# Optimization experiments

Measured on AMD Instinct MI355X. Metric: run time of the kernel, lower is better.

The kernel has to match this reference:

```python
import jax, jax.numpy as jnp
import numpy as np

B, S, DX, DM, H = 4, 2048, 1024, 1024, 16
DK = DM // H


def setup_inputs() -> dict:
    key = jax.random.key(0)
    ks = jax.random.split(key, 12)
    s = 0.02
    inp = {
        "q": jax.random.normal(ks[0], (B, S, DX), jnp.float32),
        "k": jax.random.normal(ks[1], (B, S, DX), jnp.float32),
        "v": jax.random.normal(ks[2], (B, S, DX), jnp.float32),
        "wq": jax.random.normal(ks[3], (DX, DM), jnp.float32) * s,
        "bq": jnp.zeros((DM,), jnp.float32),
        "wk": jax.random.normal(ks[4], (DX, DM), jnp.float32) * s,
        "bk": jnp.zeros((DM,), jnp.float32),
        "wv": jax.random.normal(ks[5], (DX, DM), jnp.float32) * s,
        "bv": jnp.zeros((DM,), jnp.float32),
        "wo": jax.random.normal(ks[6], (DM, DX), jnp.float32) * s,
        "bo": jnp.zeros((DX,), jnp.float32),
        # causal boolean mask [B, S_q, S_k]; True = attend
        "mask": jnp.broadcast_to(jnp.tril(jnp.ones((S, S), bool)), (B, S, S)),
    }
    return inp


def reference(q, k, v, wq, bq, wk, bk, wv, bv, wo, bo, mask):
    # Linear projections: [B,S,DX] @ [DX,DM] -> [B,S,DM]
    qh = (q @ wq + bq).reshape(B, S, H, DK).transpose(0, 2, 1, 3)  # [B,H,S,DK]
    kh = (k @ wk + bk).reshape(B, S, H, DK).transpose(0, 2, 1, 3)
    vh = (v @ wv + bv).reshape(B, S, H, DK).transpose(0, 2, 1, 3)

    scores = jnp.einsum("bhqd,bhkd->bhqk", qh, kh) / jnp.sqrt(jnp.float32(DK))
    neg = -jnp.finfo(scores.dtype).max
    scores = jnp.where(mask[:, None, :, :], scores, neg)  # mask.unsqueeze(1)
    p = jax.nn.softmax(scores, axis=-1)  # dropout inactive (eval / p=0)
    z = jnp.einsum("bhqk,bhkd->bhqd", p, vh)  # [B,H,S,DK]
    z = z.transpose(0, 2, 1, 3).reshape(B, S, DM)
    return z @ wo + bo
```

## Files before the change

### kernel.cpp

```cpp
#include <hip/hip_runtime.h>
#include <hip/hip_bf16.h>
#include <cstdint>

constexpr int Bb = 4, Sq = 2048, DXc = 1024, DMc = 1024, NH = 16, DKc = 64;
constexpr int GM = Bb * Sq;

typedef __attribute__((ext_vector_type(8))) short short8;
typedef __attribute__((ext_vector_type(4))) float f32x4;

__device__ inline float b2f(unsigned short u) {
  union { float f; uint32_t i; } c; c.i = ((uint32_t)u) << 16; return c.f;
}
__device__ inline unsigned short f2b(float f) {
  union { float f; uint32_t i; } c; c.f = f;
  uint32_t lsb = (c.i >> 16) & 1;
  c.i += 0x7fffu + lsb;
  return (unsigned short)(c.i >> 16);
}

__device__ inline void load16_lds(const unsigned short* g, unsigned short* l) {
  __builtin_amdgcn_global_load_lds(
      (const __attribute__((address_space(1))) void*)g,
      (__attribute__((address_space(3))) void*)l, 16, 0, 0);
}

__global__ __launch_bounds__(256) void cvt_k(const float* __restrict__ in,
                                             unsigned short* __restrict__ out,
                                             int n4) {
  const int i = blockIdx.x * 256 + threadIdx.x;
  if (i < n4) {
    float4 v = ((const float4*)in)[i];
    ushort4 o;
    o.x = f2b(v.x); o.y = f2b(v.y); o.z = f2b(v.z); o.w = f2b(v.w);
    ((ushort4*)out)[i] = o;
  }
}

__global__ __launch_bounds__(256) void wt_k(const float* __restrict__ W,
                                            unsigned short* __restrict__ WT) {
  __shared__ float t[64][65];
  const int tid = threadIdx.x;
  const int k0 = blockIdx.y * 64, n0 = blockIdx.x * 64;
#pragma unroll
  for (int p = 0; p < 4; ++p) {
    const int c = tid + p * 256;
    const int r = c >> 4, c4 = (c & 15) << 2;
    float4 v = *(const float4*)&W[(size_t)(k0 + r) * 1024 + n0 + c4];
    t[r][c4 + 0] = v.x; t[r][c4 + 1] = v.y; t[r][c4 + 2] = v.z; t[r][c4 + 3] = v.w;
  }
  __syncthreads();
#pragma unroll
  for (int p = 0; p < 4; ++p) {
    const int c = tid + p * 256;
    const int n = c >> 4, k4 = (c & 15) << 2;
    ushort4 o;
    o.x = f2b(t[k4 + 0][n]); o.y = f2b(t[k4 + 1][n]);
    o.z = f2b(t[k4 + 2][n]); o.w = f2b(t[k4 + 3][n]);
    *(ushort4*)&WT[(size_t)(n0 + n) * 1024 + k0 + k4] = o;
  }
}

template <int MODE>
__global__ __launch_bounds__(256) void mgemm_k(
    const unsigned short* __restrict__ A,
    const unsigned short* __restrict__ BT,
    const float* __restrict__ bias,
    float* __restrict__ outF, unsigned short* __restrict__ outB) {
  constexpr int K = 1024;
  __shared__ __align__(16) unsigned short As[128 * 32];
  __shared__ __align__(16) unsigned short Bs[128 * 32];
  const int tid = threadIdx.x;
  const int lane = tid & 63;
  const int quad = lane >> 4, l16 = lane & 15;
  const int w = tid >> 6;
  const int wrow = (w >> 1) * 64, wcol = (w & 1) * 64;
  const int m0 = blockIdx.y * 128, n0 = blockIdx.x * 128;

  f32x4 acc[4][4];
#pragma unroll
  for (int i = 0; i < 4; ++i)
#pragma unroll
    for (int j = 0; j < 4; ++j) acc[i][j] = (f32x4){0.f, 0.f, 0.f, 0.f};

  for (int k0 = 0; k0 < K; k0 += 32) {
    __syncthreads();
#pragma unroll
    for (int p = 0; p < 2; ++p) {
      const int c = tid + p * 256;
      const int row = c >> 2, ks = (c & 3) << 3;
      load16_lds(&A[(size_t)(m0 + row) * K + k0 + ks], &As[c * 8]);
      load16_lds(&BT[(size_t)(n0 + row) * K + k0 + ks], &Bs[c * 8]);
    }
    __syncthreads();

    short8 af[4], bf[4];
#pragma unroll
    for (int i = 0; i < 4; ++i)
      af[i] = *(const short8*)&As[(wrow + i * 16 + l16) * 32 + quad * 8];
#pragma unroll
    for (int j = 0; j < 4; ++j)
      bf[j] = *(const short8*)&Bs[(wcol + j * 16 + l16) * 32 + quad * 8];
#pragma unroll
    for (int i = 0; i < 4; ++i)
#pragma unroll
      for (int j = 0; j < 4; ++j)
        acc[i][j] = __builtin_amdgcn_mfma_f32_16x16x32_bf16(af[i], bf[j], acc[i][j], 0, 0, 0);
  }

  float bv[4];
#pragma unroll
  for (int j = 0; j < 4; ++j) bv[j] = bias[n0 + wcol + j * 16 + l16];
#pragma unroll
  for (int i = 0; i < 4; ++i)
#pragma unroll
    for (int j = 0; j < 4; ++j)
#pragma unroll
      for (int r = 0; r < 4; ++r) {
        const int m = m0 + wrow + i * 16 + quad * 4 + r;
        const int n = n0 + wcol + j * 16 + l16;
        const float v = acc[i][j][r] + bv[j];
        if (MODE == 0) {
          outF[(size_t)m * 1024 + n] = v;
        } else if (MODE == 1) {
          const int b = m >> 11, s = m & 2047, h = n >> 6, d = n & 63;
          outB[(((size_t)(b * NH + h) * Sq + s) << 6) + d] = f2b(v);
        } else {
          const int b = m >> 11, s = m & 2047, h = n >> 6, d = n & 63;
          outB[(((size_t)(b * NH + h) * DKc + d) << 11) + s] = f2b(v);
        }
      }
}

__global__ __launch_bounds__(512) void flash_k(
    const unsigned short* __restrict__ Qh, const unsigned short* __restrict__ Kh,
    const unsigned short* __restrict__ Vt, unsigned short* __restrict__ Zb) {
  constexpr int LDP = 72;
  __shared__ __align__(16) unsigned short Klds[64 * 64];
  __shared__ __align__(16) unsigned short Vlds[64 * 64];
  __shared__ __align__(16) unsigned short Plds[8 * 16 * LDP];
  const int tid = threadIdx.x;
  const int w = tid >> 6, lane = tid & 63;
  const int quad = lane >> 4, l16 = lane & 15;
  const int bh = blockIdx.x & 63;
  const int qi = blockIdx.x >> 6;
  const int qa = qi * 128;
  const int qbv = (15 - qi) * 128;
  const size_t base = (size_t)bh * Sq * DKc;
  unsigned short* Pw = &Plds[w * 16 * LDP];

  const int qb[2] = {qa + w * 16, qbv + (7 - w) * 16};
  const int tiles_s[2] = {2 * qi + 1 + (w >= 4 ? 1 : 0),
                          31 - 2 * qi + (w < 4 ? 1 : 0)};
  const int ntile = 32 - 2 * qi;

  short8 qf0[2], qf1[2];
#pragma unroll
  for (int s = 0; s < 2; ++s) {
    const unsigned short* qp = Qh + base + (size_t)(qb[s] + l16) * DKc + quad * 8;
    qf0[s] = *(const short8*)qp;
    qf1[s] = *(const short8*)(qp + 32);
  }

  f32x4 oacc[2][4];
#pragma unroll
  for (int s = 0; s < 2; ++s)
#pragma unroll
    for (int n = 0; n < 4; ++n) oacc[s][n] = (f32x4){0.f, 0.f, 0.f, 0.f};
  float lsum[2] = {0.f, 0.f};

  const int row0 = tid >> 3, sp0 = tid & 7, gs0 = sp0 ^ (row0 & 7);
  const int pos0 = quad ^ (l16 & 7);
  const int pos1 = pos0 ^ 4;

  for (int it = 0; it < ntile; ++it) {
    const int kt0 = it * 64;
    __syncthreads();
    load16_lds(Kh + base + (size_t)(kt0 + row0) * DKc + gs0 * 8, &Klds[tid * 8]);
    load16_lds(Vt + base + (size_t)row0 * Sq + kt0 + gs0 * 8, &Vlds[tid * 8]);
    __syncthreads();

    short8 kf0[4], kf1[4];
#pragma unroll
    for (int t = 0; t < 4; ++t) {
      const int krow = (t * 16 + l16) * 64;
      kf0[t] = *(const short8*)&Klds[krow + pos0 * 8];
      kf1[t] = *(const short8*)&Klds[krow + pos1 * 8];
    }

#pragma unroll
    for (int s = 0; s < 2; ++s) {
      if (it >= tiles_s[s]) continue;
      f32x4 st[4];
#pragma unroll
      for (int t = 0; t < 4; ++t) {
        f32x4 z4 = (f32x4){0.f, 0.f, 0.f, 0.f};
        z4 = __builtin_amdgcn_mfma_f32_16x16x32_bf16(kf0[t], qf0[s], z4, 0, 0, 0);
        st[t] = __builtin_amdgcn_mfma_f32_16x16x32_bf16(kf1[t], qf1[s], z4, 0, 0, 0);
      }
      const int qrow = qb[s] + l16;
      float p[4][4];
      if (it == tiles_s[s] - 1) {
#pragma unroll
        for (int t = 0; t < 4; ++t)
#pragma unroll
          for (int r = 0; r < 4; ++r) {
            const int key = kt0 + t * 16 + quad * 4 + r;
            const float e = __expf(fminf(st[t][r] * 0.125f, 30.f));
            p[t][r] = (key <= qrow) ? e : 0.f;
          }
      } else {
#pragma unroll
        for (int t = 0; t < 4; ++t)
#pragma unroll
          for (int r = 0; r < 4; ++r)
            p[t][r] = __expf(fminf(st[t][r] * 0.125f, 30.f));
      }
#pragma unroll
      for (int t = 0; t < 4; ++t)
#pragma unroll
        for (int r = 0; r < 4; ++r) lsum[s] += p[t][r];
#pragma unroll
      for (int t = 0; t < 4; ++t) {
        ushort4 pk;
        pk.x = f2b(p[t][0]); pk.y = f2b(p[t][1]);
        pk.z = f2b(p[t][2]); pk.w = f2b(p[t][3]);
        *(ushort4*)&Pw[l16 * LDP + t * 16 + quad * 4] = pk;
      }
      short8 pf0 = *(const short8*)&Pw[l16 * LDP + quad * 8];
      short8 pf1 = *(const short8*)&Pw[l16 * LDP + 32 + quad * 8];
#pragma unroll
      for (int n = 0; n < 4; ++n) {
        const int vrow = (n * 16 + l16) * 64;
        short8 vf0 = *(const short8*)&Vlds[vrow + pos0 * 8];
        short8 vf1 = *(const short8*)&Vlds[vrow + pos1 * 8];
        oacc[s][n] = __builtin_amdgcn_mfma_f32_16x16x32_bf16(pf0, vf0, oacc[s][n], 0, 0, 0);
        oacc[s][n] = __builtin_amdgcn_mfma_f32_16x16x32_bf16(pf1, vf1, oacc[s][n], 0, 0, 0);
      }
    }
  }

  const int b = bh >> 4, h = bh & 15;
#pragma unroll
  for (int s = 0; s < 2; ++s) {
    float ls = lsum[s];
    ls += __shfl_xor(ls, 16, 64);
    ls += __shfl_xor(ls, 32, 64);
    const float inv = 1.f / ls;
    float invr[4];
#pragma unroll
    for (int r = 0; r < 4; ++r) invr[r] = __shfl(inv, quad * 4 + r, 64);
#pragma unroll
    for (int r = 0; r < 4; ++r) {
      const int row = qb[s] + quad * 4 + r;
      unsigned short* zp = Zb + ((size_t)b * Sq + row) * DMc + h * 64;
#pragma unroll
      for (int n = 0; n < 4; ++n) zp[n * 16 + l16] = f2b(oacc[s][n][r] * invr[r]);
    }
  }
}

extern "C" void kernel_launch(void* const* d_in, const int* in_sizes, int n_in,
                              void* d_out, int out_size, void* d_ws, size_t ws_size,
                              hipStream_t stream) {
  const float* q  = (const float*)d_in[0];
  const float* k  = (const float*)d_in[1];
  const float* v  = (const float*)d_in[2];
  const float* wq = (const float*)d_in[3];
  const float* bq = (const float*)d_in[4];
  const float* wk = (const float*)d_in[5];
  const float* bk = (const float*)d_in[6];
  const float* wv = (const float*)d_in[7];
  const float* bv = (const float*)d_in[8];
  const float* wo = (const float*)d_in[9];
  const float* bo = (const float*)d_in[10];

  constexpr size_t NEL = (size_t)GM * DMc;
  unsigned short* qh  = (unsigned short*)d_ws;
  unsigned short* kh  = qh + NEL;
  unsigned short* vh  = kh + NEL;
  unsigned short* xbf = vh + NEL;
  unsigned short* wqt = xbf + NEL;
  unsigned short* wkt = wqt + (size_t)DXc * DMc;
  unsigned short* wvt = wkt + (size_t)DXc * DMc;
  unsigned short* wot = wvt + (size_t)DXc * DMc;

  const dim3 tgrid(16, 16);
  wt_k<<<tgrid, 256, 0, stream>>>(wq, wqt);
  wt_k<<<tgrid, 256, 0, stream>>>(wk, wkt);
  wt_k<<<tgrid, 256, 0, stream>>>(wv, wvt);
  wt_k<<<tgrid, 256, 0, stream>>>(wo, wot);

  const int n4 = (int)(NEL / 4);
  const dim3 ggrid(DMc / 128, GM / 128);
  cvt_k<<<(n4 + 255) / 256, 256, 0, stream>>>(q, xbf, n4);
  mgemm_k<1><<<ggrid, 256, 0, stream>>>(xbf, wqt, bq, nullptr, qh);
  cvt_k<<<(n4 + 255) / 256, 256, 0, stream>>>(k, xbf, n4);
  mgemm_k<1><<<ggrid, 256, 0, stream>>>(xbf, wkt, bk, nullptr, kh);
  cvt_k<<<(n4 + 255) / 256, 256, 0, stream>>>(v, xbf, n4);
  mgemm_k<2><<<ggrid, 256, 0, stream>>>(xbf, wvt, bv, nullptr, vh);

  flash_k<<<dim3(512), 512, 0, stream>>>(qh, kh, vh, xbf);
  mgemm_k<0><<<ggrid, 256, 0, stream>>>(xbf, wot, bo, (float*)d_out, nullptr);
}
```

Before: 392.5 us.

## Fuse fp32-to-bf16 conversion into batched QKV GEMM and prefetch flash K/V tiles

Removes the separate input conversion kernels by loading fp32 activations directly in the projection GEMM and packing them to bf16 with v_cvt_pk_bf16_f32 before staging in LDS. The three QKV projections and four weight transposes are each batched into one launch via blockIdx.z. The flash kernel now register-prefetches the next K/V tile during compute instead of using direct global-to-LDS loads. This cuts launches and fp32 round-trips through memory, at the cost of synchronous fp32 A loads inside the GEMM main loop and different LDS swizzle handling.

```diff
diff --git a/kernel.cpp b/kernel.cpp
--- a/kernel.cpp
+++ b/kernel.cpp
@@ -8,9 +8,6 @@
 typedef __attribute__((ext_vector_type(8))) short short8;
 typedef __attribute__((ext_vector_type(4))) float f32x4;
 
-__device__ inline float b2f(unsigned short u) {
-  union { float f; uint32_t i; } c; c.i = ((uint32_t)u) << 16; return c.f;
-}
 __device__ inline unsigned short f2b(float f) {
   union { float f; uint32_t i; } c; c.f = f;
   uint32_t lsb = (c.i >> 16) & 1;
@@ -18,26 +15,26 @@
   return (unsigned short)(c.i >> 16);
 }
 
+__device__ inline uint32_t cvt_pk_bf16(float lo, float hi) {
+  uint32_t r;
+  asm("v_cvt_pk_bf16_f32 %0, %1, %2" : "=v"(r) : "v"(lo), "v"(hi));
+  return r;
+}
+
 __device__ inline void load16_lds(const unsigned short* g, unsigned short* l) {
   __builtin_amdgcn_global_load_lds(
       (const __attribute__((address_space(1))) void*)g,
       (__attribute__((address_space(3))) void*)l, 16, 0, 0);
 }
 
-__global__ __launch_bounds__(256) void cvt_k(const float* __restrict__ in,
-                                             unsigned short* __restrict__ out,
-                                             int n4) {
-  const int i = blockIdx.x * 256 + threadIdx.x;
-  if (i < n4) {
-    float4 v = ((const float4*)in)[i];
-    ushort4 o;
-    o.x = f2b(v.x); o.y = f2b(v.y); o.z = f2b(v.z); o.w = f2b(v.w);
-    ((ushort4*)out)[i] = o;
-  }
-}
-
-__global__ __launch_bounds__(256) void wt_k(const float* __restrict__ W,
-                                            unsigned short* __restrict__ WT) {
+__global__ __launch_bounds__(256) void wt4_k(
+    const float* __restrict__ wq, const float* __restrict__ wk,
+    const float* __restrict__ wv, const float* __restrict__ wo,
+    unsigned short* __restrict__ wqt, unsigned short* __restrict__ wkt,
+    unsigned short* __restrict__ wvt, unsigned short* __restrict__ wot) {
+  const int z = blockIdx.z;
+  const float* W = z == 0 ? wq : z == 1 ? wk : z == 2 ? wv : wo;
+  unsigned short* WT = z == 0 ? wqt : z == 1 ? wkt : z == 2 ? wvt : wot;
   __shared__ float t[64][65];
   const int tid = threadIdx.x;
   const int k0 = blockIdx.y * 64, n0 = blockIdx.x * 64;
@@ -60,12 +57,102 @@
   }
 }
 
-template <int MODE>
-__global__ __launch_bounds__(256) void mgemm_k(
-    const unsigned short* __restrict__ A,
-    const unsigned short* __restrict__ BT,
-    const float* __restrict__ bias,
-    float* __restrict__ outF, unsigned short* __restrict__ outB) {
+__global__ __launch_bounds__(256) void qkv_k(
+    const float* __restrict__ q, const float* __restrict__ k,
+    const float* __restrict__ v,
+    const unsigned short* __restrict__ wqt, const unsigned short* __restrict__ wkt,
+    const unsigned short* __restrict__ wvt,
+    const float* __restrict__ bq, const float* __restrict__ bk,
+    const float* __restrict__ bv,
+    unsigned short* __restrict__ qh, unsigned short* __restrict__ kh,
+    unsigned short* __restrict__ vh) {
+  constexpr int K = 1024;
+  __shared__ __align__(16) unsigned short As[128 * 32];
+  __shared__ __align__(16) unsigned short Bs[128 * 32];
+  const int z = blockIdx.z;
+  const float* A = z == 0 ? q : z == 1 ? k : v;
+  const unsigned short* BT = z == 0 ? wqt : z == 1 ? wkt : wvt;
+  const float* bias = z == 0 ? bq : z == 1 ? bk : bv;
+  unsigned short* outB = z == 0 ? qh : z == 1 ? kh : vh;
+
+  const int tid = threadIdx.x;
+  const int lane = tid & 63;
+  const int quad = lane >> 4, l16 = lane & 15;
+  const int w = tid >> 6;
+  const int wrow = (w >> 1) * 64, wcol = (w & 1) * 64;
+  const int m0 = blockIdx.y * 128, n0 = blockIdx.x * 128;
+
+  const int s0 = tid, s1 = tid + 256;
+  const int ar0 = s0 >> 2, ac0 = (s0 & 3) * 8;
+  const int ar1 = s1 >> 2, ac1 = (s1 & 3) * 8;
+
+  f32x4 acc[4][4];
+#pragma unroll
+  for (int i = 0; i < 4; ++i)
+#pragma unroll
+    for (int j = 0; j < 4; ++j) acc[i][j] = (f32x4){0.f, 0.f, 0.f, 0.f};
+
+  for (int k0 = 0; k0 < K; k0 += 32) {
+    __syncthreads();
+#pragma unroll
+    for (int p = 0; p < 2; ++p) {
+      const int c = tid + p * 256;
+      const int row = c >> 2, ks = (c & 3) << 3;
+      load16_lds(&BT[(size_t)(n0 + row) * K + k0 + ks], &Bs[c * 8]);
+    }
+    const float4 a0 = *(const float4*)&A[(size_t)(m0 + ar0) * K + k0 + ac0];
+    const float4 a1 = *(const float4*)&A[(size_t)(m0 + ar0) * K + k0 + ac0 + 4];
+    const float4 a2 = *(const float4*)&A[(size_t)(m0 + ar1) * K + k0 + ac1];
+    const float4 a3 = *(const float4*)&A[(size_t)(m0 + ar1) * K + k0 + ac1 + 4];
+    {
+      uint4 p0, p1;
+      p0.x = cvt_pk_bf16(a0.x, a0.y); p0.y = cvt_pk_bf16(a0.z, a0.w);
+      p0.z = cvt_pk_bf16(a1.x, a1.y); p0.w = cvt_pk_bf16(a1.z, a1.w);
+      p1.x = cvt_pk_bf16(a2.x, a2.y); p1.y = cvt_pk_bf16(a2.z, a2.w);
+      p1.z = cvt_pk_bf16(a3.x, a3.y); p1.w = cvt_pk_bf16(a3.z, a3.w);
+      *(uint4*)&As[s0 * 8] = p0;
+      *(uint4*)&As[s1 * 8] = p1;
+    }
+    __syncthreads();
+
+    short8 af[4], bf[4];
+#pragma unroll
+    for (int i = 0; i < 4; ++i)
+      af[i] = *(const short8*)&As[(wrow + i * 16 + l16) * 32 + quad * 8];
+#pragma unroll
+    for (int j = 0; j < 4; ++j)
+      bf[j] = *(const short8*)&Bs[(wcol + j * 16 + l16) * 32 + quad * 8];
+#pragma unroll
+    for (int i = 0; i < 4; ++i)
+#pragma unroll
+      for (int j = 0; j < 4; ++j)
+        acc[i][j] = __builtin_amdgcn_mfma_f32_16x16x32_bf16(af[i], bf[j], acc[i][j], 0, 0, 0);
+  }
+
+  float bvv[4];
+#pragma unroll
+  for (int j = 0; j < 4; ++j) bvv[j] = bias[n0 + wcol + j * 16 + l16];
+#pragma unroll
+  for (int i = 0; i < 4; ++i)
+#pragma unroll
+    for (int j = 0; j < 4; ++j)
+#pragma unroll
+      for (int r = 0; r < 4; ++r) {
+        const int m = m0 + wrow + i * 16 + quad * 4 + r;
+        const int n = n0 + wcol + j * 16 + l16;
+        const float val = acc[i][j][r] + bvv[j];
+        const int b = m >> 11, s = m & 2047, h = n >> 6, d = n & 63;
+        if (z < 2) {
+          outB[(((size_t)(b * NH + h) * Sq + s) << 6) + d] = f2b(val);
+        } else {
+          outB[(((size_t)(b * NH + h) * DKc + d) << 11) + s] = f2b(val);
+        }
+      }
+}
+
+__global__ __launch_bounds__(256) void mgemm_o(
+    const unsigned short* __restrict__ A, const unsigned short* __restrict__ BT,
+    const float* __restrict__ bias, float* __restrict__ outF) {
   constexpr int K = 1024;
   __shared__ __align__(16) unsigned short As[128 * 32];
   __shared__ __align__(16) unsigned short Bs[128 * 32];
@@ -118,16 +205,7 @@
       for (int r = 0; r < 4; ++r) {
         const int m = m0 + wrow + i * 16 + quad * 4 + r;
         const int n = n0 + wcol + j * 16 + l16;
-        const float v = acc[i][j][r] + bv[j];
-        if (MODE == 0) {
-          outF[(size_t)m * 1024 + n] = v;
-        } else if (MODE == 1) {
-          const int b = m >> 11, s = m & 2047, h = n >> 6, d = n & 63;
-          outB[(((size_t)(b * NH + h) * Sq + s) << 6) + d] = f2b(v);
-        } else {
-          const int b = m >> 11, s = m & 2047, h = n >> 6, d = n & 63;
-          outB[(((size_t)(b * NH + h) * DKc + d) << 11) + s] = f2b(v);
-        }
+        outF[(size_t)m * 1024 + n] = acc[i][j][r] + bv[j];
       }
 }
 
@@ -168,15 +246,25 @@
     for (int n = 0; n < 4; ++n) oacc[s][n] = (f32x4){0.f, 0.f, 0.f, 0.f};
   float lsum[2] = {0.f, 0.f};
 
-  const int row0 = tid >> 3, sp0 = tid & 7, gs0 = sp0 ^ (row0 & 7);
+  const int row0 = tid >> 3, sp0 = tid & 7;
+  const int xseg = sp0 ^ (row0 & 7);
+  const int dst = (row0 * 8 + xseg) * 8;
   const int pos0 = quad ^ (l16 & 7);
   const int pos1 = pos0 ^ 4;
 
+  uint4 kreg = *(const uint4*)(Kh + base + (size_t)row0 * DKc + sp0 * 8);
+  uint4 vreg = *(const uint4*)(Vt + base + (size_t)row0 * Sq + sp0 * 8);
+
   for (int it = 0; it < ntile; ++it) {
     const int kt0 = it * 64;
     __syncthreads();
-    load16_lds(Kh + base + (size_t)(kt0 + row0) * DKc + gs0 * 8, &Klds[tid * 8]);
-    load16_lds(Vt + base + (size_t)row0 * Sq + kt0 + gs0 * 8, &Vlds[tid * 8]);
+    *(uint4*)&Klds[dst] = kreg;
+    *(uint4*)&Vlds[dst] = vreg;
+    if (it + 1 < ntile) {
+      const int kn = kt0 + 64;
+      kreg = *(const uint4*)(Kh + base + (size_t)(kn + row0) * DKc + sp0 * 8);
+      vreg = *(const uint4*)(Vt + base + (size_t)row0 * Sq + kn + sp0 * 8);
+    }
     __syncthreads();
 
     short8 kf0[4], kf1[4];
@@ -284,21 +372,9 @@
   unsigned short* wvt = wkt + (size_t)DXc * DMc;
   unsigned short* wot = wvt + (size_t)DXc * DMc;
 
-  const dim3 tgrid(16, 16);
-  wt_k<<<tgrid, 256, 0, stream>>>(wq, wqt);
-  wt_k<<<tgrid, 256, 0, stream>>>(wk, wkt);
-  wt_k<<<tgrid, 256, 0, stream>>>(wv, wvt);
-  wt_k<<<tgrid, 256, 0, stream>>>(wo, wot);
-
-  const int n4 = (int)(NEL / 4);
-  const dim3 ggrid(DMc / 128, GM / 128);
-  cvt_k<<<(n4 + 255) / 256, 256, 0, stream>>>(q, xbf, n4);
-  mgemm_k<1><<<ggrid, 256, 0, stream>>>(xbf, wqt, bq, nullptr, qh);
-  cvt_k<<<(n4 + 255) / 256, 256, 0, stream>>>(k, xbf, n4);
-  mgemm_k<1><<<ggrid, 256, 0, stream>>>(xbf, wkt, bk, nullptr, kh);
-  cvt_k<<<(n4 + 255) / 256, 256, 0, stream>>>(v, xbf, n4);
-  mgemm_k<2><<<ggrid, 256, 0, stream>>>(xbf, wvt, bv, nullptr, vh);
-
+  wt4_k<<<dim3(16, 16, 4), 256, 0, stream>>>(wq, wk, wv, wo, wqt, wkt, wvt, wot);
+  qkv_k<<<dim3(8, 64, 3), 256, 0, stream>>>(q, k, v, wqt, wkt, wvt,
+                                            bq, bk, bv, qh, kh, vh);
   flash_k<<<dim3(512), 512, 0, stream>>>(qh, kh, vh, xbf);
-  mgemm_k<0><<<ggrid, 256, 0, stream>>>(xbf, wot, bo, (float*)d_out, nullptr);
-}
+  mgemm_o<<<dim3(8, 64), 256, 0, stream>>>(xbf, wot, bo, (float*)d_out);
+}
```

Measured after the change: 395.2 us. Within noise of the previous version (+0.7%).
